# Optimization experiments

Measured on AMD Instinct MI355X. Metric: run time of the kernel, lower is better.

The kernel has to match this reference:

```python
import math
import jax, jax.numpy as jnp
import numpy as np

B, S, D, H = 2, 2048, 1024, 16
HD = D // H


def setup_inputs() -> dict:
    key = jax.random.key(0)
    ks = jax.random.split(key, 12)
    w = lambda k: jax.random.normal(k, (D, D), jnp.float32) * 0.02
    return {
        "query": jax.random.normal(ks[0], (B, S, D), jnp.float32),
        "key": jax.random.normal(ks[1], (B, S, D), jnp.float32),
        "value": jax.random.normal(ks[2], (B, S, D), jnp.float32),
        "mask": jax.random.randint(ks[3], (B, 1, S, S), 0, 2, jnp.int32),
        "relative_pos_bias": jax.random.normal(ks[4], (S, S, H), jnp.float32) * 0.1,
        "Wq": w(ks[5]), "bq": jnp.zeros((D,), jnp.float32),
        "Wk": w(ks[6]), "bk": jnp.zeros((D,), jnp.float32),
        "Wv": w(ks[7]), "bv": jnp.zeros((D,), jnp.float32),
        "Wo": w(ks[8]), "bo": jnp.zeros((D,), jnp.float32),
    }


def reference(query, key, value, mask, relative_pos_bias,
              Wq, bq, Wk, bk, Wv, bv, Wo, bo):
    b, s, d = query.shape
    h = relative_pos_bias.shape[-1]
    hd = d // h
    scale = math.sqrt(hd)
    # projections -> (b, h, s, hd)
    split = lambda x: x.reshape(b, s, h, hd).transpose(0, 2, 1, 3)
    Q = split(query @ Wq + bq)
    K = split(key @ Wk + bk)
    V = split(value @ Wv + bv)
    scores = jnp.einsum("bhqd,bhkd->bhqk", Q, K) / scale
    # torch: bias.unsqueeze(0).transpose(1,3) => scores[b,h,i,j] += bias[j,i,h]
    scores = scores + jnp.transpose(relative_pos_bias, (2, 1, 0))[None]
    scores = jnp.where(mask == 0, jnp.float32(-1e9), scores)
    attn = jax.nn.softmax(scores, axis=-1)
    out = jnp.einsum("bhqk,bhkd->bhqd", attn, V)
    out = out.transpose(0, 2, 1, 3).reshape(b, s, d)
    return out @ Wo + bo
```

## Files before the change

### kernel.cpp

```cpp
#include <hip/hip_runtime.h>
#include <math.h>

#define SS 2048
#define DD 1024
#define HH 16

typedef _Float16 f16;
typedef _Float16 half8 __attribute__((ext_vector_type(8)));
typedef float f32x4 __attribute__((ext_vector_type(4)));
typedef unsigned long long u64;

#define LOG2E 1.44269504f
#define MASKNEG -30000.0f

__device__ __forceinline__ void gload16(const void* g, void* lds) {
    __builtin_amdgcn_global_load_lds(
        (const __attribute__((address_space(1))) unsigned int*)g,
        (__attribute__((address_space(3))) unsigned int*)lds, 16, 0, 0);
}

__device__ __forceinline__ float dpp_max16(float x) {
    float y;
    y = __uint_as_float(__builtin_amdgcn_mov_dpp(__float_as_uint(x), 0xB1, 0xF, 0xF, false));
    x = fmaxf(x, y);
    y = __uint_as_float(__builtin_amdgcn_mov_dpp(__float_as_uint(x), 0x4E, 0xF, 0xF, false));
    x = fmaxf(x, y);
    y = __uint_as_float(__builtin_amdgcn_mov_dpp(__float_as_uint(x), 0x124, 0xF, 0xF, false));
    x = fmaxf(x, y);
    y = __uint_as_float(__builtin_amdgcn_mov_dpp(__float_as_uint(x), 0x128, 0xF, 0xF, false));
    x = fmaxf(x, y);
    return x;
}
__device__ __forceinline__ float dpp_sum16(float x) {
    float y;
    y = __uint_as_float(__builtin_amdgcn_mov_dpp(__float_as_uint(x), 0xB1, 0xF, 0xF, false));
    x += y;
    y = __uint_as_float(__builtin_amdgcn_mov_dpp(__float_as_uint(x), 0x4E, 0xF, 0xF, false));
    x += y;
    y = __uint_as_float(__builtin_amdgcn_mov_dpp(__float_as_uint(x), 0x124, 0xF, 0xF, false));
    x += y;
    y = __uint_as_float(__builtin_amdgcn_mov_dpp(__float_as_uint(x), 0x128, 0xF, 0xF, false));
    x += y;
    return x;
}

__global__ __launch_bounds__(256)
void cvt_x(const float* __restrict__ q, const float* __restrict__ k,
           const float* __restrict__ v, f16* __restrict__ oq,
           f16* __restrict__ ok, f16* __restrict__ ov)
{
    const int z = blockIdx.z;
    const float* src = z == 0 ? q : z == 1 ? k : v;
    f16* dst = z == 0 ? oq : z == 1 ? ok : ov;
    size_t i = ((size_t)blockIdx.x * 256 + threadIdx.x) * 8;
    float4 v0 = *reinterpret_cast<const float4*>(src + i);
    float4 v1 = *reinterpret_cast<const float4*>(src + i + 4);
    half8 h;
    h[0] = (f16)v0.x; h[1] = (f16)v0.y; h[2] = (f16)v0.z; h[3] = (f16)v0.w;
    h[4] = (f16)v1.x; h[5] = (f16)v1.y; h[6] = (f16)v1.z; h[7] = (f16)v1.w;
    *reinterpret_cast<half8*>(dst + i) = h;
}

__global__ __launch_bounds__(256)
void cvt_wT(const float* __restrict__ wq, const float* __restrict__ wk,
            const float* __restrict__ wv, const float* __restrict__ wo,
            f16* __restrict__ oq, f16* __restrict__ ok,
            f16* __restrict__ ov, f16* __restrict__ oo)
{
    __shared__ float Lt[64][65];
    const int z = blockIdx.z;
    const float* W = z == 0 ? wq : z == 1 ? wk : z == 2 ? wv : wo;
    f16* WT = z == 0 ? oq : z == 1 ? ok : z == 2 ? ov : oo;
    const int n0 = blockIdx.x * 64, k0 = blockIdx.y * 64;
    const int t = threadIdx.x;
    {
        int row = t >> 2;
        int c0  = (t & 3) * 16;
#pragma unroll
        for (int u = 0; u < 4; ++u) {
            float4 x = *reinterpret_cast<const float4*>(
                &W[(size_t)(k0 + row) * DD + n0 + c0 + u * 4]);
            Lt[row][c0 + u * 4 + 0] = x.x;
            Lt[row][c0 + u * 4 + 1] = x.y;
            Lt[row][c0 + u * 4 + 2] = x.z;
            Lt[row][c0 + u * 4 + 3] = x.w;
        }
    }
    __syncthreads();
    {
        int n  = t >> 2;
        int kc = (t & 3) * 16;
        half8 h0, h1;
#pragma unroll
        for (int u = 0; u < 8; ++u) h0[u] = (f16)Lt[kc + u][n];
#pragma unroll
        for (int u = 0; u < 8; ++u) h1[u] = (f16)Lt[kc + 8 + u][n];
        f16* dst = &WT[(size_t)(n0 + n) * DD + k0 + kc];
        *reinterpret_cast<half8*>(dst) = h0;
        *reinterpret_cast<half8*>(dst + 8) = h1;
    }
}

__global__ __launch_bounds__(256)
void cvt_rpbT(const float* __restrict__ rpb, f16* __restrict__ rpbT)
{
    __shared__ f16 Lt[16][16][66];
    const int t = threadIdx.x, wid = t >> 6, l = t & 63;
    const int i0 = blockIdx.x * 16;
    const int j0 = blockIdx.y * 64;
    const int il = l >> 2;
    const int h0 = (l & 3) * 4;
#pragma unroll
    for (int p = 0; p < 16; ++p) {
        int jl = p * 4 + wid;
        float4 v = *reinterpret_cast<const float4*>(
            rpb + ((size_t)(j0 + jl) * SS + i0 + il) * HH + h0);
        Lt[h0 + 0][il][jl] = (f16)(v.x * LOG2E);
        Lt[h0 + 1][il][jl] = (f16)(v.y * LOG2E);
        Lt[h0 + 2][il][jl] = (f16)(v.z * LOG2E);
        Lt[h0 + 3][il][jl] = (f16)(v.w * LOG2E);
    }
    __syncthreads();
    const int part = t & 7;
#pragma unroll
    for (int p = 0; p < 8; ++p) {
        int rowid = p * 32 + (t >> 3);
        int h = rowid >> 4, i2 = rowid & 15;
        half8 v = *reinterpret_cast<const half8*>(&Lt[h][i2][part * 8]);
        *reinterpret_cast<half8*>(
            rpbT + ((size_t)h * SS + i0 + i2) * SS + j0 + part * 8) = v;
    }
}

__global__ __launch_bounds__(256)
void cvt_maskbits(const int* __restrict__ mask, u64* __restrict__ mb)
{
    const int t = threadIdx.x, wid = t >> 6, l = t & 63;
    const int row = blockIdx.x * 4 + wid;
    const int* src = mask + (size_t)row * SS;
    u64* dst = mb + (size_t)row * 32;
    for (int it = 0; it < 32; ++it) {
        int mv = src[it * 64 + l];
        u64 bal = __ballot(mv != 0);
        if (l == 0) dst[it] = bal;
    }
}

__global__ __launch_bounds__(256)
void proj3(const f16* __restrict__ Xq, const f16* __restrict__ Xk,
           const f16* __restrict__ Xv, const f16* __restrict__ WqT,
           const f16* __restrict__ WkT, const f16* __restrict__ WvT,
           const float* __restrict__ bq, const float* __restrict__ bk,
           const float* __restrict__ bv,
           f16* __restrict__ Qo, f16* __restrict__ Ko, f16* __restrict__ VTo)
{
    __shared__ f16 As[128 * 64];
    __shared__ f16 Bs[128 * 64];
    const int t = threadIdx.x, wid = t >> 6, l = t & 63, c = l & 15, g = l >> 4;
    const int gz = blockIdx.z;
    const f16 *Ap, *Bp; const float* bias; int m0, n0;
    if (gz == 2) { Ap = WvT; Bp = Xv; bias = bv; m0 = blockIdx.x * 128; n0 = blockIdx.y * 128; }
    else if (gz == 1) { Ap = Xk; Bp = WkT; bias = bk; m0 = blockIdx.y * 128; n0 = blockIdx.x * 128; }
    else { Ap = Xq; Bp = WqT; bias = bq; m0 = blockIdx.y * 128; n0 = blockIdx.x * 128; }
    const int wm = wid >> 1, wn = wid & 1;
    f32x4 acc[4][4] = {};
    char* AsB = (char*)As; char* BsB = (char*)Bs;

    for (int k0 = 0; k0 < DD; k0 += 64) {
        __syncthreads();
#pragma unroll
        for (int j = 0; j < 4; ++j) {
            int row = wid * 32 + j * 8 + (l >> 3);
            int slot = (l & 7) ^ (row & 7);
            gload16(Ap + (size_t)(m0 + row) * DD + k0 + slot * 8,
                    AsB + (wid * 32 + j * 8) * 128);
            gload16(Bp + (size_t)(n0 + row) * DD + k0 + slot * 8,
                    BsB + (wid * 32 + j * 8) * 128);
        }
        __syncthreads();
#pragma unroll
        for (int ks = 0; ks < 2; ++ks) {
            half8 af[4];
#pragma unroll
            for (int mt = 0; mt < 4; ++mt) {
                int row = wm * 64 + mt * 16 + c;
                af[mt] = *(const half8*)(AsB + row * 128 +
                         ((ks * 64 + g * 16) ^ ((row & 7) << 4)));
            }
#pragma unroll
            for (int nt = 0; nt < 4; ++nt) {
                int row = wn * 64 + nt * 16 + c;
                half8 bf = *(const half8*)(BsB + row * 128 +
                           ((ks * 64 + g * 16) ^ ((row & 7) << 4)));
#pragma unroll
                for (int mt = 0; mt < 4; ++mt)
                    acc[mt][nt] = __builtin_amdgcn_mfma_f32_16x16x32_f16(
                        af[mt], bf, acc[mt][nt], 0, 0, 0);
            }
        }
    }

    const float post = (gz == 0) ? 0.125f * LOG2E : 1.0f;
    if (gz < 2) {
        f16* dst = gz ? Ko : Qo;
#pragma unroll
        for (int nt = 0; nt < 4; ++nt) {
            int n = n0 + wn * 64 + nt * 16 + c;
            float bn = bias[n];
            int h = n >> 6, hd = n & 63;
#pragma unroll
            for (int mt = 0; mt < 4; ++mt)
#pragma unroll
                for (int reg = 0; reg < 4; ++reg) {
                    int m = m0 + wm * 64 + mt * 16 + 4 * g + reg;
                    int b = m >> 11, s = m & (SS - 1);
                    dst[(((size_t)(b * HH + h)) * SS + s) * 64 + hd] =
                        (f16)((acc[mt][nt][reg] + bn) * post);
                }
        }
    } else {
#pragma unroll
        for (int mt = 0; mt < 4; ++mt)
#pragma unroll
            for (int reg = 0; reg < 4; ++reg) {
                int m = m0 + wm * 64 + mt * 16 + 4 * g + reg;
                float bd = bias[m];
                int h = m >> 6, dl = m & 63;
#pragma unroll
                for (int nt = 0; nt < 4; ++nt) {
                    int n = n0 + wn * 64 + nt * 16 + c;
                    int b = n >> 11, s = n & (SS - 1);
                    VTo[(((size_t)(b * HH + h)) * 64 + dl) * SS + s] =
                        (f16)(acc[mt][nt][reg] + bd);
                }
            }
    }
}

__global__ __launch_bounds__(256, 4)
void attn_fwd(const f16* __restrict__ Qw, const f16* __restrict__ Kw,
              const f16* __restrict__ VTw, const f16* __restrict__ rpbT,
              const u64* __restrict__ mbits, f16* __restrict__ AOh)
{
    __shared__ f16 Qs[64 * 64];
    __shared__ f16 Ks[2][64 * 64];
    __shared__ f16 Vs[2][64 * 64];
    char* QsB = (char*)Qs;

    const int t = threadIdx.x, wid = t >> 6, l = t & 63, c = l & 15, g = l >> 4;
    const int bh = blockIdx.x, b = bh >> 4, h = bh & 15;
    const int q0 = blockIdx.y * 64;
    const size_t baseSD = (size_t)bh * SS * 64;
    const size_t baseDS = (size_t)bh * 64 * SS;
    const f16* Kbase = Kw + baseSD;
    const f16* Vbase = VTw + baseDS;
    const f16* rpbH = rpbT + (size_t)h * SS * SS;

    const f16* biasRow[4];
    const u64* mbRow[4];
#pragma unroll
    for (int reg = 0; reg < 4; ++reg) {
        int qrow = q0 + wid * 16 + 4 * g + reg;
        biasRow[reg] = rpbH + (size_t)qrow * SS + c;
        mbRow[reg]   = mbits + ((size_t)b * SS + qrow) * 32;
    }

    const int srow0 = wid * 16 + (l >> 3);
    const int ke    = (l & 7) * 8;
    const int sswz  = (srow0 & 7) << 4;
    const int sdst  = ((l & 7) << 4) ^ sswz;

#pragma unroll
    for (int j = 0; j < 2; ++j) {
        int row = wid * 16 + j * 8 + (l >> 3);
        int slot = (l & 7) ^ (row & 7);
        gload16(Qw + baseSD + (size_t)(q0 + row) * 64 + slot * 8,
                QsB + (wid * 16 + j * 8) * 128);
    }
    {
        half8 k0 = *(const half8*)(Kbase + (size_t)srow0 * 64 + ke);
        half8 k1 = *(const half8*)(Kbase + (size_t)(srow0 + 8) * 64 + ke);
        half8 v0 = *(const half8*)(Vbase + (size_t)srow0 * SS + ke);
        half8 v1 = *(const half8*)(Vbase + (size_t)(srow0 + 8) * SS + ke);
        char* kd = (char*)Ks[0]; char* vd = (char*)Vs[0];
        *(half8*)(kd + srow0 * 128 + sdst) = k0;
        *(half8*)(kd + (srow0 + 8) * 128 + sdst) = k1;
        *(half8*)(vd + srow0 * 128 + sdst) = v0;
        *(half8*)(vd + (srow0 + 8) * 128 + sdst) = v1;
    }
    f16 bb[4][4]; u64 mm[4];
#pragma unroll
    for (int reg = 0; reg < 4; ++reg) {
#pragma unroll
        for (int nt = 0; nt < 4; ++nt) bb[reg][nt] = biasRow[reg][nt * 16];
        mm[reg] = mbRow[reg][0];
    }
    __syncthreads();

    half8 qf[2];
    f32x4 acc_o[4] = {};
    float mrow[4], lp[4];
#pragma unroll
    for (int r = 0; r < 4; ++r) { mrow[r] = -INFINITY; lp[r] = 0.f; }

    int buf = 0;
    for (int kt = 0; kt < SS / 64; ++kt) {
        const bool more = (kt + 1 < SS / 64);
        const int jn = more ? (kt + 1) * 64 : 0;
        const int ktn = more ? kt + 1 : 0;

        half8 k0n = *(const half8*)(Kbase + (size_t)(jn + srow0) * 64 + ke);
        half8 k1n = *(const half8*)(Kbase + (size_t)(jn + srow0 + 8) * 64 + ke);
        half8 v0n = *(const half8*)(Vbase + (size_t)srow0 * SS + jn + ke);
        half8 v1n = *(const half8*)(Vbase + (size_t)(srow0 + 8) * SS + jn + ke);
        f16 bbn[4][4]; u64 mmn[4];
#pragma unroll
        for (int reg = 0; reg < 4; ++reg) {
#pragma unroll
            for (int nt = 0; nt < 4; ++nt) bbn[reg][nt] = biasRow[reg][jn + nt * 16];
            mmn[reg] = mbRow[reg][ktn];
        }

        char* KsB = (char*)Ks[buf];
        char* VsB = (char*)Vs[buf];
        if (kt == 0) {
#pragma unroll
            for (int ks = 0; ks < 2; ++ks) {
                int row = wid * 16 + c;
                qf[ks] = *(const half8*)(QsB + row * 128 +
                         ((ks * 64 + g * 16) ^ ((row & 7) << 4)));
            }
        }
        f32x4 sc[4] = {};
#pragma unroll
        for (int ks = 0; ks < 2; ++ks)
#pragma unroll
            for (int nt = 0; nt < 4; ++nt) {
                int row = nt * 16 + c;
                half8 kf = *(const half8*)(KsB + row * 128 +
                           ((ks * 64 + g * 16) ^ ((row & 7) << 4)));
                sc[nt] = __builtin_amdgcn_mfma_f32_16x16x32_f16(
                    qf[ks], kf, sc[nt], 0, 0, 0);
            }
#pragma unroll
        for (int reg = 0; reg < 4; ++reg) {
            u64 sh = mm[reg] >> c;
            float s0 = sc[0][reg] + ((sh & 1)         ? (float)bb[reg][0] : MASKNEG);
            float s1 = sc[1][reg] + (((sh >> 16) & 1) ? (float)bb[reg][1] : MASKNEG);
            float s2 = sc[2][reg] + (((sh >> 32) & 1) ? (float)bb[reg][2] : MASKNEG);
            float s3 = sc[3][reg] + (((sh >> 48) & 1) ? (float)bb[reg][3] : MASKNEG);
            float rm = fmaxf(fmaxf(s0, s1), fmaxf(s2, s3));
            rm = dpp_max16(rm);
            float mn = fmaxf(mrow[reg], rm);
            float scal = exp2f(mrow[reg] - mn);
            mrow[reg] = mn;
            float p0 = exp2f(s0 - mn), p1 = exp2f(s1 - mn);
            float p2 = exp2f(s2 - mn), p3 = exp2f(s3 - mn);
            sc[0][reg] = p0; sc[1][reg] = p1;
            sc[2][reg] = p2; sc[3][reg] = p3;
            lp[reg] = lp[reg] * scal + (p0 + p1 + p2 + p3);
#pragma unroll
            for (int nt = 0; nt < 4; ++nt) acc_o[nt][reg] *= scal;
        }
#pragma unroll
        for (int reg = 0; reg < 4; ++reg) {
            int qrl = wid * 16 + 4 * g + reg;
            char* pr = QsB + qrl * 128;
            int sw = (qrl & 7) << 4;
#pragma unroll
            for (int nt = 0; nt < 4; ++nt)
                *(f16*)(pr + ((nt * 32 + c * 2) ^ sw)) = (f16)sc[nt][reg];
        }
#pragma unroll
        for (int ks = 0; ks < 2; ++ks) {
            int prow = wid * 16 + c;
            half8 pa = *(const half8*)(QsB + prow * 128 +
                       ((ks * 64 + g * 16) ^ ((prow & 7) << 4)));
#pragma unroll
            for (int nt = 0; nt < 4; ++nt) {
                int row = nt * 16 + c;
                half8 vf = *(const half8*)(VsB + row * 128 +
                           ((ks * 64 + g * 16) ^ ((row & 7) << 4)));
                acc_o[nt] = __builtin_amdgcn_mfma_f32_16x16x32_f16(
                    pa, vf, acc_o[nt], 0, 0, 0);
            }
        }
        if (more) {
            char* kd = (char*)Ks[buf ^ 1];
            char* vd = (char*)Vs[buf ^ 1];
            *(half8*)(kd + srow0 * 128 + sdst) = k0n;
            *(half8*)(kd + (srow0 + 8) * 128 + sdst) = k1n;
            *(half8*)(vd + srow0 * 128 + sdst) = v0n;
            *(half8*)(vd + (srow0 + 8) * 128 + sdst) = v1n;
            buf ^= 1;
#pragma unroll
            for (int reg = 0; reg < 4; ++reg) {
#pragma unroll
                for (int nt = 0; nt < 4; ++nt) bb[reg][nt] = bbn[reg][nt];
                mm[reg] = mmn[reg];
            }
        }
        __syncthreads();
    }
#pragma unroll
    for (int reg = 0; reg < 4; ++reg) {
        float lrow = dpp_sum16(lp[reg]);
        float inv = 1.0f / lrow;
        int qrow = q0 + wid * 16 + 4 * g + reg;
#pragma unroll
        for (int nt = 0; nt < 4; ++nt)
            AOh[((size_t)b * SS + qrow) * DD + h * 64 + nt * 16 + c] =
                (f16)(acc_o[nt][reg] * inv);
    }
}

__global__ __launch_bounds__(256)
void gemm_out(const f16* __restrict__ A, const f16* __restrict__ BT,
              const float* __restrict__ bias, float* __restrict__ out)
{
    __shared__ f16 As[128 * 64];
    __shared__ f16 Bs[128 * 64];
    const int t = threadIdx.x, wid = t >> 6, l = t & 63, c = l & 15, g = l >> 4;
    const int m0 = blockIdx.y * 128, n0 = blockIdx.x * 128;
    const int wm = wid >> 1, wn = wid & 1;
    f32x4 acc[4][4] = {};
    char* AsB = (char*)As; char* BsB = (char*)Bs;

    for (int k0 = 0; k0 < DD; k0 += 64) {
        __syncthreads();
#pragma unroll
        for (int j = 0; j < 4; ++j) {
            int row = wid * 32 + j * 8 + (l >> 3);
            int slot = (l & 7) ^ (row & 7);
            gload16(A + (size_t)(m0 + row) * DD + k0 + slot * 8,
                    AsB + (wid * 32 + j * 8) * 128);
            gload16(BT + (size_t)(n0 + row) * DD + k0 + slot * 8,
                    BsB + (wid * 32 + j * 8) * 128);
        }
        __syncthreads();
#pragma unroll
        for (int ks = 0; ks < 2; ++ks) {
            half8 af[4];
#pragma unroll
            for (int mt = 0; mt < 4; ++mt) {
                int row = wm * 64 + mt * 16 + c;
                af[mt] = *(const half8*)(AsB + row * 128 +
                         ((ks * 64 + g * 16) ^ ((row & 7) << 4)));
            }
#pragma unroll
            for (int nt = 0; nt < 4; ++nt) {
                int row = wn * 64 + nt * 16 + c;
                half8 bf = *(const half8*)(BsB + row * 128 +
                           ((ks * 64 + g * 16) ^ ((row & 7) << 4)));
#pragma unroll
                for (int mt = 0; mt < 4; ++mt)
                    acc[mt][nt] = __builtin_amdgcn_mfma_f32_16x16x32_f16(
                        af[mt], bf, acc[mt][nt], 0, 0, 0);
            }
        }
    }
#pragma unroll
    for (int nt = 0; nt < 4; ++nt) {
        int n = n0 + wn * 64 + nt * 16 + c;
        float bn = bias[n];
#pragma unroll
        for (int mt = 0; mt < 4; ++mt)
#pragma unroll
            for (int reg = 0; reg < 4; ++reg) {
                int m = m0 + wm * 64 + mt * 16 + 4 * g + reg;
                out[(size_t)m * DD + n] = acc[mt][nt][reg] + bn;
            }
    }
}

extern "C" void kernel_launch(void* const* d_in, const int* in_sizes, int n_in,
                              void* d_out, int out_size, void* d_ws, size_t ws_size,
                              hipStream_t stream)
{
    (void)in_sizes; (void)n_in; (void)out_size; (void)ws_size;

    const float* query = (const float*)d_in[0];
    const float* key   = (const float*)d_in[1];
    const float* value = (const float*)d_in[2];
    const int*   mask  = (const int*)d_in[3];
    const float* rpb   = (const float*)d_in[4];
    const float* Wq = (const float*)d_in[5];  const float* bq = (const float*)d_in[6];
    const float* Wk = (const float*)d_in[7];  const float* bk = (const float*)d_in[8];
    const float* Wv = (const float*)d_in[9];  const float* bv = (const float*)d_in[10];
    const float* Wo = (const float*)d_in[11]; const float* bo = (const float*)d_in[12];
    float* out = (float*)d_out;

    const size_t NX = (size_t)2 * SS * DD;
    const size_t NW = (size_t)DD * DD;
    f16* Xq    = (f16*)d_ws;
    f16* Xk    = Xq + NX;
    f16* Xv    = Xk + NX;
    f16* WqT   = Xv + NX;
    f16* WkT   = WqT + NW;
    f16* WvT   = WkT + NW;
    f16* WoT   = WvT + NW;
    f16* Qw    = WoT + NW;
    f16* Kw    = Qw + NX;
    f16* VTw   = Kw + NX;
    f16* rpbT  = VTw + NX;
    u64* mbits = (u64*)(rpbT + (size_t)HH * SS * SS);
    f16* AOh   = Xq;

    cvt_x<<<dim3(NX / 2048, 1, 3), 256, 0, stream>>>(query, key, value, Xq, Xk, Xv);
    cvt_wT<<<dim3(16, 16, 4), 256, 0, stream>>>(Wq, Wk, Wv, Wo, WqT, WkT, WvT, WoT);
    cvt_rpbT<<<dim3(SS / 16, SS / 64), 256, 0, stream>>>(rpb, rpbT);
    cvt_maskbits<<<dim3((2 * SS) / 4), 256, 0, stream>>>(mask, mbits);
    proj3<<<dim3(8, 32, 3), 256, 0, stream>>>(Xq, Xk, Xv, WqT, WkT, WvT,
                                              bq, bk, bv, Qw, Kw, VTw);
    attn_fwd<<<dim3(2 * HH, SS / 64), 256, 0, stream>>>(Qw, Kw, VTw, rpbT, mbits, AOh);
    gemm_out<<<dim3(8, 32), 256, 0, stream>>>(AOh, WoT, bo, out);
}
```

Measured before the change: 332.3 us.

## Compute transposed S=K·Q^T in attention to keep P in registers

Rewrites the attention inner loop so scores are computed as K·Q^T. Each lane then holds a query column, and the softmax probabilities feed the PV MFMA straight from registers via 16x16x16 instructions, with no trip through LDS. The bias table and V tile are stored in a permuted column order to match the new register layout. Q is loaded directly into registers, mask and bias are folded into the accumulator init, and the running-max rescale is skipped unless the max grows by more than a threshold. s_setprio is also raised around the MFMA blocks. This removes LDS traffic and some barriers, at the cost of more complex index permutations and a lazy-rescale heuristic that could affect numerical accuracy.

```diff
diff --git a/kernel.cpp b/kernel.cpp
--- a/kernel.cpp
+++ b/kernel.cpp
@@ -7,6 +7,7 @@
 
 typedef _Float16 f16;
 typedef _Float16 half8 __attribute__((ext_vector_type(8)));
+typedef _Float16 half4 __attribute__((ext_vector_type(4)));
 typedef float f32x4 __attribute__((ext_vector_type(4)));
 typedef unsigned long long u64;
 
@@ -17,31 +18,6 @@
     __builtin_amdgcn_global_load_lds(
         (const __attribute__((address_space(1))) unsigned int*)g,
         (__attribute__((address_space(3))) unsigned int*)lds, 16, 0, 0);
-}
-
-__device__ __forceinline__ float dpp_max16(float x) {
-    float y;
-    y = __uint_as_float(__builtin_amdgcn_mov_dpp(__float_as_uint(x), 0xB1, 0xF, 0xF, false));
-    x = fmaxf(x, y);
-    y = __uint_as_float(__builtin_amdgcn_mov_dpp(__float_as_uint(x), 0x4E, 0xF, 0xF, false));
-    x = fmaxf(x, y);
-    y = __uint_as_float(__builtin_amdgcn_mov_dpp(__float_as_uint(x), 0x124, 0xF, 0xF, false));
-    x = fmaxf(x, y);
-    y = __uint_as_float(__builtin_amdgcn_mov_dpp(__float_as_uint(x), 0x128, 0xF, 0xF, false));
-    x = fmaxf(x, y);
-    return x;
-}
-__device__ __forceinline__ float dpp_sum16(float x) {
-    float y;
-    y = __uint_as_float(__builtin_amdgcn_mov_dpp(__float_as_uint(x), 0xB1, 0xF, 0xF, false));
-    x += y;
-    y = __uint_as_float(__builtin_amdgcn_mov_dpp(__float_as_uint(x), 0x4E, 0xF, 0xF, false));
-    x += y;
-    y = __uint_as_float(__builtin_amdgcn_mov_dpp(__float_as_uint(x), 0x124, 0xF, 0xF, false));
-    x += y;
-    y = __uint_as_float(__builtin_amdgcn_mov_dpp(__float_as_uint(x), 0x128, 0xF, 0xF, false));
-    x += y;
-    return x;
 }
 
 __global__ __launch_bounds__(256)
@@ -102,7 +78,7 @@
 }
 
 __global__ __launch_bounds__(256)
-void cvt_rpbT(const float* __restrict__ rpb, f16* __restrict__ rpbT)
+void cvt_rpbT3(const float* __restrict__ rpb, f16* __restrict__ rpbT)
 {
     __shared__ f16 Lt[16][16][66];
     const int t = threadIdx.x, wid = t >> 6, l = t & 63;
@@ -126,7 +102,12 @@
     for (int p = 0; p < 8; ++p) {
         int rowid = p * 32 + (t >> 3);
         int h = rowid >> 4, i2 = rowid & 15;
-        half8 v = *reinterpret_cast<const half8*>(&Lt[h][i2][part * 8]);
+        half8 v;
+#pragma unroll
+        for (int e = 0; e < 8; ++e) {
+            int sig = 32 * (part & 1) + 16 * (e >> 2) + 4 * (part >> 1) + (e & 3);
+            v[e] = Lt[h][i2][sig];
+        }
         *reinterpret_cast<half8*>(
             rpbT + ((size_t)h * SS + i0 + i2) * SS + j0 + part * 8) = v;
     }
@@ -242,10 +223,8 @@
               const f16* __restrict__ VTw, const f16* __restrict__ rpbT,
               const u64* __restrict__ mbits, f16* __restrict__ AOh)
 {
-    __shared__ f16 Qs[64 * 64];
     __shared__ f16 Ks[2][64 * 64];
     __shared__ f16 Vs[2][64 * 64];
-    char* QsB = (char*)Qs;
 
     const int t = threadIdx.x, wid = t >> 6, l = t & 63, c = l & 15, g = l >> 4;
     const int bh = blockIdx.x, b = bh >> 4, h = bh & 15;
@@ -254,54 +233,50 @@
     const size_t baseDS = (size_t)bh * 64 * SS;
     const f16* Kbase = Kw + baseSD;
     const f16* Vbase = VTw + baseDS;
-    const f16* rpbH = rpbT + (size_t)h * SS * SS;
-
-    const f16* biasRow[4];
-    const u64* mbRow[4];
-#pragma unroll
-    for (int reg = 0; reg < 4; ++reg) {
-        int qrow = q0 + wid * 16 + 4 * g + reg;
-        biasRow[reg] = rpbH + (size_t)qrow * SS + c;
-        mbRow[reg]   = mbits + ((size_t)b * SS + qrow) * 32;
-    }
-
+
+    const int qrow_c = q0 + wid * 16 + c;
+    const f16* bp = rpbT + (size_t)h * SS * SS + (size_t)qrow_c * SS + g * 16;
+    const u64* mp = mbits + ((size_t)b * SS + qrow_c) * 32;
+
+    const int s     = l & 7;
     const int srow0 = wid * 16 + (l >> 3);
-    const int ke    = (l & 7) * 8;
     const int sswz  = (srow0 & 7) << 4;
-    const int sdst  = ((l & 7) << 4) ^ sswz;
-
-#pragma unroll
-    for (int j = 0; j < 2; ++j) {
-        int row = wid * 16 + j * 8 + (l >> 3);
-        int slot = (l & 7) ^ (row & 7);
-        gload16(Qw + baseSD + (size_t)(q0 + row) * 64 + slot * 8,
-                QsB + (wid * 16 + j * 8) * 128);
-    }
+    const int kdst  = (s << 4) ^ sswz;
+    const int velo  = 32 * (s >> 2) + 16 * (s & 1) + 4 * ((s >> 1) & 1);
+    const int vdlo  = (velo * 2) ^ sswz;
+    const int vdhi  = (velo * 2 + 16) ^ sswz;
+
+    int ga[4];
+#pragma unroll
+    for (int r = 0; r < 4; ++r) ga[r] = (g * 4 + r) * 4;
+
+    half8 qf[2];
+    qf[0] = *(const half8*)(Qw + baseSD + (size_t)qrow_c * 64 + g * 8);
+    qf[1] = *(const half8*)(Qw + baseSD + (size_t)qrow_c * 64 + 32 + g * 8);
+
     {
-        half8 k0 = *(const half8*)(Kbase + (size_t)srow0 * 64 + ke);
-        half8 k1 = *(const half8*)(Kbase + (size_t)(srow0 + 8) * 64 + ke);
-        half8 v0 = *(const half8*)(Vbase + (size_t)srow0 * SS + ke);
-        half8 v1 = *(const half8*)(Vbase + (size_t)(srow0 + 8) * SS + ke);
+        half8 k0 = *(const half8*)(Kbase + (size_t)srow0 * 64 + s * 8);
+        half8 k1 = *(const half8*)(Kbase + (size_t)(srow0 + 8) * 64 + s * 8);
+        half8 v0 = *(const half8*)(Vbase + (size_t)srow0 * SS + s * 8);
+        half8 v1 = *(const half8*)(Vbase + (size_t)(srow0 + 8) * SS + s * 8);
         char* kd = (char*)Ks[0]; char* vd = (char*)Vs[0];
-        *(half8*)(kd + srow0 * 128 + sdst) = k0;
-        *(half8*)(kd + (srow0 + 8) * 128 + sdst) = k1;
-        *(half8*)(vd + srow0 * 128 + sdst) = v0;
-        *(half8*)(vd + (srow0 + 8) * 128 + sdst) = v1;
-    }
-    f16 bb[4][4]; u64 mm[4];
-#pragma unroll
-    for (int reg = 0; reg < 4; ++reg) {
-#pragma unroll
-        for (int nt = 0; nt < 4; ++nt) bb[reg][nt] = biasRow[reg][nt * 16];
-        mm[reg] = mbRow[reg][0];
-    }
+        *(half8*)(kd + srow0 * 128 + kdst) = k0;
+        *(half8*)(kd + (srow0 + 8) * 128 + kdst) = k1;
+        half4 lo0 = {v0[0], v0[1], v0[2], v0[3]}, hi0 = {v0[4], v0[5], v0[6], v0[7]};
+        half4 lo1 = {v1[0], v1[1], v1[2], v1[3]}, hi1 = {v1[4], v1[5], v1[6], v1[7]};
+        *(half4*)(vd + srow0 * 128 + vdlo) = lo0;
+        *(half4*)(vd + srow0 * 128 + vdhi) = hi0;
+        *(half4*)(vd + (srow0 + 8) * 128 + vdlo) = lo1;
+        *(half4*)(vd + (srow0 + 8) * 128 + vdhi) = hi1;
+    }
+    half8 bb0 = *(const half8*)(bp);
+    half8 bb1 = *(const half8*)(bp + 8);
+    u64 mm = mp[0];
     __syncthreads();
 
-    half8 qf[2];
-    f32x4 acc_o[4] = {};
-    float mrow[4], lp[4];
-#pragma unroll
-    for (int r = 0; r < 4; ++r) { mrow[r] = -INFINITY; lp[r] = 0.f; }
+    f32x4 acc[4] = {};
+    float mrow = -INFINITY, lp = 0.f;
+    const int shg = 4 * g;
 
     int buf = 0;
     for (int kt = 0; kt < SS / 64; ++kt) {
@@ -309,29 +284,28 @@
         const int jn = more ? (kt + 1) * 64 : 0;
         const int ktn = more ? kt + 1 : 0;
 
-        half8 k0n = *(const half8*)(Kbase + (size_t)(jn + srow0) * 64 + ke);
-        half8 k1n = *(const half8*)(Kbase + (size_t)(jn + srow0 + 8) * 64 + ke);
-        half8 v0n = *(const half8*)(Vbase + (size_t)srow0 * SS + jn + ke);
-        half8 v1n = *(const half8*)(Vbase + (size_t)(srow0 + 8) * SS + jn + ke);
-        f16 bbn[4][4]; u64 mmn[4];
-#pragma unroll
-        for (int reg = 0; reg < 4; ++reg) {
-#pragma unroll
-            for (int nt = 0; nt < 4; ++nt) bbn[reg][nt] = biasRow[reg][jn + nt * 16];
-            mmn[reg] = mbRow[reg][ktn];
-        }
+        half8 k0n = *(const half8*)(Kbase + (size_t)(jn + srow0) * 64 + s * 8);
+        half8 k1n = *(const half8*)(Kbase + (size_t)(jn + srow0 + 8) * 64 + s * 8);
+        half8 v0n = *(const half8*)(Vbase + (size_t)srow0 * SS + jn + s * 8);
+        half8 v1n = *(const half8*)(Vbase + (size_t)(srow0 + 8) * SS + jn + s * 8);
+        half8 bbn0 = *(const half8*)(bp + jn);
+        half8 bbn1 = *(const half8*)(bp + jn + 8);
+        u64 mmn = mp[ktn];
 
         char* KsB = (char*)Ks[buf];
         char* VsB = (char*)Vs[buf];
-        if (kt == 0) {
-#pragma unroll
-            for (int ks = 0; ks < 2; ++ks) {
-                int row = wid * 16 + c;
-                qf[ks] = *(const half8*)(QsB + row * 128 +
-                         ((ks * 64 + g * 16) ^ ((row & 7) << 4)));
-            }
-        }
-        f32x4 sc[4] = {};
+
+        u64 sh = mm >> shg;
+        f32x4 sc[4];
+#pragma unroll
+        for (int nt = 0; nt < 4; ++nt)
+#pragma unroll
+            for (int r = 0; r < 4; ++r) {
+                float bf = (float)(nt < 2 ? bb0[nt * 4 + r] : bb1[(nt - 2) * 4 + r]);
+                sc[nt][r] = ((sh >> (16 * nt + r)) & 1) ? bf : MASKNEG;
+            }
+
+        __builtin_amdgcn_s_setprio(1);
 #pragma unroll
         for (int ks = 0; ks < 2; ++ks)
 #pragma unroll
@@ -340,77 +314,99 @@
                 half8 kf = *(const half8*)(KsB + row * 128 +
                            ((ks * 64 + g * 16) ^ ((row & 7) << 4)));
                 sc[nt] = __builtin_amdgcn_mfma_f32_16x16x32_f16(
-                    qf[ks], kf, sc[nt], 0, 0, 0);
-            }
-#pragma unroll
-        for (int reg = 0; reg < 4; ++reg) {
-            u64 sh = mm[reg] >> c;
-            float s0 = sc[0][reg] + ((sh & 1)         ? (float)bb[reg][0] : MASKNEG);
-            float s1 = sc[1][reg] + (((sh >> 16) & 1) ? (float)bb[reg][1] : MASKNEG);
-            float s2 = sc[2][reg] + (((sh >> 32) & 1) ? (float)bb[reg][2] : MASKNEG);
-            float s3 = sc[3][reg] + (((sh >> 48) & 1) ? (float)bb[reg][3] : MASKNEG);
-            float rm = fmaxf(fmaxf(s0, s1), fmaxf(s2, s3));
-            rm = dpp_max16(rm);
-            float mn = fmaxf(mrow[reg], rm);
-            float scal = exp2f(mrow[reg] - mn);
-            mrow[reg] = mn;
-            float p0 = exp2f(s0 - mn), p1 = exp2f(s1 - mn);
-            float p2 = exp2f(s2 - mn), p3 = exp2f(s3 - mn);
-            sc[0][reg] = p0; sc[1][reg] = p1;
-            sc[2][reg] = p2; sc[3][reg] = p3;
-            lp[reg] = lp[reg] * scal + (p0 + p1 + p2 + p3);
-#pragma unroll
-            for (int nt = 0; nt < 4; ++nt) acc_o[nt][reg] *= scal;
-        }
-#pragma unroll
-        for (int reg = 0; reg < 4; ++reg) {
-            int qrl = wid * 16 + 4 * g + reg;
-            char* pr = QsB + qrl * 128;
-            int sw = (qrl & 7) << 4;
+                    kf, qf[ks], sc[nt], 0, 0, 0);
+            }
+        __builtin_amdgcn_s_setprio(0);
+
+        float rm = fmaxf(fmaxf(fmaxf(sc[0][0], sc[0][1]), fmaxf(sc[0][2], sc[0][3])),
+                         fmaxf(fmaxf(sc[1][0], sc[1][1]), fmaxf(sc[1][2], sc[1][3])));
+        rm = fmaxf(rm, fmaxf(fmaxf(fmaxf(sc[2][0], sc[2][1]), fmaxf(sc[2][2], sc[2][3])),
+                             fmaxf(fmaxf(sc[3][0], sc[3][1]), fmaxf(sc[3][2], sc[3][3]))));
+        rm = fmaxf(rm, __shfl_xor(rm, 16));
+        rm = fmaxf(rm, __shfl_xor(rm, 32));
+        if (!__all(rm <= mrow + 8.0f)) {
+            float mn = fmaxf(mrow, rm);
+            float scal = exp2f(mrow - mn);
+            mrow = mn;
+            lp *= scal;
+            float sq[4];
+#pragma unroll
+            for (int r = 0; r < 4; ++r)
+                sq[r] = __int_as_float(__builtin_amdgcn_ds_bpermute(
+                            ga[r], __float_as_int(scal)));
 #pragma unroll
             for (int nt = 0; nt < 4; ++nt)
-                *(f16*)(pr + ((nt * 32 + c * 2) ^ sw)) = (f16)sc[nt][reg];
-        }
-#pragma unroll
-        for (int ks = 0; ks < 2; ++ks) {
-            int prow = wid * 16 + c;
-            half8 pa = *(const half8*)(QsB + prow * 128 +
-                       ((ks * 64 + g * 16) ^ ((prow & 7) << 4)));
-#pragma unroll
-            for (int nt = 0; nt < 4; ++nt) {
-                int row = nt * 16 + c;
+#pragma unroll
+                for (int r = 0; r < 4; ++r) acc[nt][r] *= sq[r];
+        }
+        float psum = 0.f;
+#pragma unroll
+        for (int nt = 0; nt < 4; ++nt)
+#pragma unroll
+            for (int r = 0; r < 4; ++r) {
+                float p = exp2f(sc[nt][r] - mrow);
+                sc[nt][r] = p;
+                psum += p;
+            }
+        lp += psum;
+
+        half4 pa[4];
+#pragma unroll
+        for (int kk = 0; kk < 4; ++kk) {
+            half4 pv = {(f16)sc[kk][0], (f16)sc[kk][1],
+                        (f16)sc[kk][2], (f16)sc[kk][3]};
+            pa[kk] = pv;
+        }
+
+        __builtin_amdgcn_s_setprio(1);
+#pragma unroll
+        for (int ks = 0; ks < 2; ++ks)
+#pragma unroll
+            for (int nt2 = 0; nt2 < 4; ++nt2) {
+                int row = nt2 * 16 + c;
                 half8 vf = *(const half8*)(VsB + row * 128 +
                            ((ks * 64 + g * 16) ^ ((row & 7) << 4)));
-                acc_o[nt] = __builtin_amdgcn_mfma_f32_16x16x32_f16(
-                    pa, vf, acc_o[nt], 0, 0, 0);
-            }
-        }
+                half4 vlo = {vf[0], vf[1], vf[2], vf[3]};
+                half4 vhi = {vf[4], vf[5], vf[6], vf[7]};
+                acc[nt2] = __builtin_amdgcn_mfma_f32_16x16x16f16(
+                    pa[2 * ks], vlo, acc[nt2], 0, 0, 0);
+                acc[nt2] = __builtin_amdgcn_mfma_f32_16x16x16f16(
+                    pa[2 * ks + 1], vhi, acc[nt2], 0, 0, 0);
+            }
+        __builtin_amdgcn_s_setprio(0);
+
         if (more) {
             char* kd = (char*)Ks[buf ^ 1];
             char* vd = (char*)Vs[buf ^ 1];
-            *(half8*)(kd + srow0 * 128 + sdst) = k0n;
-            *(half8*)(kd + (srow0 + 8) * 128 + sdst) = k1n;
-            *(half8*)(vd + srow0 * 128 + sdst) = v0n;
-            *(half8*)(vd + (srow0 + 8) * 128 + sdst) = v1n;
+            *(half8*)(kd + srow0 * 128 + kdst) = k0n;
+            *(half8*)(kd + (srow0 + 8) * 128 + kdst) = k1n;
+            half4 lo0 = {v0n[0], v0n[1], v0n[2], v0n[3]}, hi0 = {v0n[4], v0n[5], v0n[6], v0n[7]};
+            half4 lo1 = {v1n[0], v1n[1], v1n[2], v1n[3]}, hi1 = {v1n[4], v1n[5], v1n[6], v1n[7]};
+            *(half4*)(vd + srow0 * 128 + vdlo) = lo0;
+            *(half4*)(vd + srow0 * 128 + vdhi) = hi0;
+            *(half4*)(vd + (srow0 + 8) * 128 + vdlo) = lo1;
+            *(half4*)(vd + (srow0 + 8) * 128 + vdhi) = hi1;
             buf ^= 1;
-#pragma unroll
-            for (int reg = 0; reg < 4; ++reg) {
-#pragma unroll
-                for (int nt = 0; nt < 4; ++nt) bb[reg][nt] = bbn[reg][nt];
-                mm[reg] = mmn[reg];
-            }
+            bb0 = bbn0; bb1 = bbn1; mm = mmn;
         }
         __syncthreads();
     }
-#pragma unroll
-    for (int reg = 0; reg < 4; ++reg) {
-        float lrow = dpp_sum16(lp[reg]);
-        float inv = 1.0f / lrow;
-        int qrow = q0 + wid * 16 + 4 * g + reg;
-#pragma unroll
-        for (int nt = 0; nt < 4; ++nt)
-            AOh[((size_t)b * SS + qrow) * DD + h * 64 + nt * 16 + c] =
-                (f16)(acc_o[nt][reg] * inv);
+
+    float lt = lp;
+    lt += __shfl_xor(lt, 16);
+    lt += __shfl_xor(lt, 32);
+    float linv[4];
+#pragma unroll
+    for (int r = 0; r < 4; ++r)
+        linv[r] = 1.0f / __int_as_float(__builtin_amdgcn_ds_bpermute(
+                      ga[r], __float_as_int(lt)));
+#pragma unroll
+    for (int r = 0; r < 4; ++r) {
+        int qrow = q0 + wid * 16 + 4 * g + r;
+#pragma unroll
+        for (int nt2 = 0; nt2 < 4; ++nt2)
+            AOh[((size_t)b * SS + qrow) * DD + h * 64 + nt2 * 16 + c] =
+                (f16)(acc[nt2][r] * linv[r]);
     }
 }
 
@@ -508,7 +504,7 @@
 
     cvt_x<<<dim3(NX / 2048, 1, 3), 256, 0, stream>>>(query, key, value, Xq, Xk, Xv);
     cvt_wT<<<dim3(16, 16, 4), 256, 0, stream>>>(Wq, Wk, Wv, Wo, WqT, WkT, WvT, WoT);
-    cvt_rpbT<<<dim3(SS / 16, SS / 64), 256, 0, stream>>>(rpb, rpbT);
+    cvt_rpbT3<<<dim3(SS / 16, SS / 64), 256, 0, stream>>>(rpb, rpbT);
     cvt_maskbits<<<dim3((2 * SS) / 4), 256, 0, stream>>>(mask, mbits);
     proj3<<<dim3(8, 32, 3), 256, 0, stream>>>(Xq, Xk, Xv, WqT, WkT, WvT,
                                               bq, bk, bv, Qw, Kw, VTw);
```

Result: faster. 297.6 us (-10.4%).
